# Performance work log

Hardware: AMD Instinct MI355X
Metric: run time of the kernel (lower is better)

The kernel has to match this reference:

```python
import jax, jax.numpy as jnp
import numpy as np

NUM_GRAPHS = 512
LEAKY_SLOPE = 0.01


def _gconv(x, src, dst, w, W_root, W_rel, b_rel):
    # PyG GraphConv: out = lin_rel(sum_j w_ij * x_j) + lin_root(x)
    msg = x[src] * w[:, None]                       # [E, d] gather + scale
    agg = jax.ops.segment_sum(msg, dst, num_segments=x.shape[0])  # scatter-add
    return agg @ W_rel + b_rel + x @ W_root


def setup_inputs() -> dict:
    key = jax.random.key(0)
    ks = jax.random.split(key, 12)
    N, E, D, H, C = 100000, 1250000, 64, 64, 8
    x_embeddings = jax.random.normal(ks[0], (N, D), dtype=jnp.float32)
    edge_index = jax.random.randint(ks[1], (2, E), 0, N, dtype=jnp.int64)
    weights = jax.random.uniform(ks[2], (E,), dtype=jnp.float32)
    batch = jnp.sort(jax.random.randint(ks[3], (N,), 0, NUM_GRAPHS, dtype=jnp.int64))
    s1 = 1.0 / np.sqrt(D)
    s2 = 1.0 / np.sqrt(H)
    W1_root = jax.random.uniform(ks[4], (D, H), jnp.float32, -s1, s1)
    W1_rel = jax.random.uniform(ks[5], (D, H), jnp.float32, -s1, s1)
    b1 = jax.random.uniform(ks[6], (H,), jnp.float32, -s1, s1)
    W2_root = jax.random.uniform(ks[7], (H, H), jnp.float32, -s2, s2)
    W2_rel = jax.random.uniform(ks[8], (H, H), jnp.float32, -s2, s2)
    b2 = jax.random.uniform(ks[9], (H,), jnp.float32, -s2, s2)
    Wl_root = jax.random.uniform(ks[10], (H, C), jnp.float32, -s2, s2)
    bl = jax.random.uniform(ks[11], (C,), jnp.float32, -s2, s2)
    return {"x_embeddings": x_embeddings, "edge_index": edge_index,
            "weights": weights, "batch": batch,
            "W1_root": W1_root, "W1_rel": W1_rel, "b1": b1,
            "W2_root": W2_root, "W2_rel": W2_rel, "b2": b2,
            "Wl_root": Wl_root, "bl": bl}


def reference(x_embeddings, edge_index, weights, batch,
              W1_root, W1_rel, b1, W2_root, W2_rel, b2, Wl_root, bl):
    src, dst = edge_index[0], edge_index[1]
    x = _gconv(x_embeddings, src, dst, weights, W1_root, W1_rel, b1)
    x = jax.nn.leaky_relu(x, LEAKY_SLOPE)
    x = _gconv(x, src, dst, weights, W2_root, W2_rel, b2)
    x = jax.nn.leaky_relu(x, LEAKY_SLOPE)
    # global_mean_pool over graph ids
    summed = jax.ops.segment_sum(x, batch, num_segments=NUM_GRAPHS)
    counts = jax.ops.segment_sum(jnp.ones((x.shape[0],), x.dtype), batch,
                                 num_segments=NUM_GRAPHS)
    pooled = summed / jnp.maximum(counts, 1.0)[:, None]
    # final GraphConv applied with no edges: agg = 0 -> W_root x + b_rel
    out = pooled @ Wl_root + bl
    return out
```

## Files before the change

### kernel.cpp

```cpp
#include <hip/hip_runtime.h>

#define LEAKY_SLOPE 0.01f
#define NUM_GRAPHS 512
#define TILE 4096
#define NB_MAX 512

typedef __attribute__((ext_vector_type(8))) short short8;
typedef __attribute__((ext_vector_type(4))) float f32x4;

static __device__ __forceinline__ unsigned short f2bf(float f) {
    unsigned u = __float_as_uint(f);
    u += 0x7FFFu + ((u >> 16) & 1u);
    return (unsigned short)(u >> 16);
}
static __device__ __forceinline__ float bf2f(unsigned short h) {
    return __uint_as_float(((unsigned)h) << 16);
}

static __device__ __forceinline__ int wave_incl_scan(int v, int lane) {
#pragma unroll
    for (int off = 1; off < 64; off <<= 1) {
        int t = __shfl_up(v, off, 64);
        if (lane >= off) v += t;
    }
    return v;
}

__global__ __launch_bounds__(256)
void p1a_hist(const int* __restrict__ dst, int* __restrict__ bucketCnt, int E, int NB) {
    __shared__ int h[NB_MAX];
    for (int t = threadIdx.x; t < NB_MAX; t += 256) h[t] = 0;
    __syncthreads();
    const int base = blockIdx.x * TILE;
#pragma unroll
    for (int i = 0; i < TILE / 256; ++i) {
        int e = base + i * 256 + threadIdx.x;
        if (e < E) atomicAdd(&h[dst[e] >> 8], 1);
    }
    __syncthreads();
    for (int t = threadIdx.x; t < NB; t += 256)
        if (h[t]) atomicAdd(&bucketCnt[t], h[t]);
}

__global__ __launch_bounds__(512)
void bscan_kernel(const int* __restrict__ bucketCnt, int* __restrict__ bucketBase,
                  int* __restrict__ cursor, int* __restrict__ rowStart,
                  int N, int E, int NB) {
    __shared__ int ws[8];
    const int t = threadIdx.x, lane = t & 63, wid = t >> 6;
    int v = (t < NB) ? bucketCnt[t] : 0;
    int s = wave_incl_scan(v, lane);
    if (lane == 63) ws[wid] = s;
    __syncthreads();
    int add = 0;
    for (int i = 0; i < wid; ++i) add += ws[i];
    if (t < NB) {
        int excl = s + add - v;
        bucketBase[t] = excl;
        cursor[t] = excl;
    }
    if (t == 0) rowStart[N] = E;
}

__global__ __launch_bounds__(256)
void p1b_partition(const int* __restrict__ src, const int* __restrict__ dst,
                   const float* __restrict__ w, int* __restrict__ cursor,
                   int2* __restrict__ tmp, int E, int NB) {
    __shared__ int h[NB_MAX];
    __shared__ int cur[NB_MAX];
    __shared__ int lstart[NB_MAX];
    __shared__ int gbase[NB_MAX];
    __shared__ int ws[4];
    __shared__ int2 pay[TILE];
    __shared__ unsigned short bk[TILE];

    for (int t = threadIdx.x; t < NB_MAX; t += 256) h[t] = 0;
    __syncthreads();

    const int base = blockIdx.x * TILE;
    int   myb[TILE / 256];
    int   myp[TILE / 256];
    float myw[TILE / 256];
#pragma unroll
    for (int i = 0; i < TILE / 256; ++i) {
        int e = base + i * 256 + threadIdx.x;
        if (e < E) {
            int d = dst[e];
            myb[i] = d >> 8;
            myp[i] = src[e] | ((d & 255) << 20);
            myw[i] = w[e];
            atomicAdd(&h[myb[i]], 1);
        } else {
            myb[i] = -1;
        }
    }
    __syncthreads();

    {
        const int t = threadIdx.x, lane = t & 63, wid = t >> 6;
        int a = h[2 * t], b = h[2 * t + 1];
        int s = wave_incl_scan(a + b, lane);
        if (lane == 63) ws[wid] = s;
        __syncthreads();
        int add = 0;
        for (int i = 0; i < wid; ++i) add += ws[i];
        int excl = s + add - (a + b);
        lstart[2 * t] = excl;
        lstart[2 * t + 1] = excl + a;
        cur[2 * t] = excl;
        cur[2 * t + 1] = excl + a;
    }
    __syncthreads();

#pragma unroll
    for (int i = 0; i < TILE / 256; ++i) {
        if (myb[i] >= 0) {
            int p = atomicAdd(&cur[myb[i]], 1);
            pay[p] = make_int2(myp[i], __float_as_int(myw[i]));
            bk[p] = (unsigned short)myb[i];
        }
    }
    __syncthreads();

    for (int t = threadIdx.x; t < NB; t += 256) {
        int c = h[t];
        if (c) gbase[t] = atomicAdd(&cursor[t], c);
    }
    __syncthreads();

    const int total = min(TILE, E - base);
    for (int s2 = threadIdx.x; s2 < total; s2 += 256) {
        int b2 = bk[s2];
        tmp[gbase[b2] + s2 - lstart[b2]] = pay[s2];
    }
}

__global__ __launch_bounds__(256)
void p2_build(const int2* __restrict__ tmp, const int* __restrict__ bucketBase,
              int* __restrict__ rowStart, int2* __restrict__ edata,
              int N, int E, int NB) {
    const int b = blockIdx.x;
    const int s = bucketBase[b];
    const int e2 = (b + 1 < NB) ? bucketBase[b + 1] : E;
    __shared__ int h[256];
    __shared__ int cur[256];
    __shared__ int ws[4];
    h[threadIdx.x] = 0;
    __syncthreads();
    for (int j = s + threadIdx.x; j < e2; j += 256) {
        int dl = (tmp[j].x >> 20) & 255;
        atomicAdd(&h[dl], 1);
    }
    __syncthreads();
    const int t = threadIdx.x, lane = t & 63, wid = t >> 6;
    int v = h[t];
    int sc = wave_incl_scan(v, lane);
    if (lane == 63) ws[wid] = sc;
    __syncthreads();
    int add = 0;
    for (int i = 0; i < wid; ++i) add += ws[i];
    int excl = sc + add - v;
    const int node = b * 256 + t;
    if (node < N) rowStart[node] = s + excl;
    cur[t] = excl;
    __syncthreads();
    for (int j = s + threadIdx.x; j < e2; j += 256) {
        int2 v2 = tmp[j];
        int dl = (v2.x >> 20) & 255;
        int p = atomicAdd(&cur[dl], 1);
        edata[s + p] = make_int2(v2.x & 0x1FFFF, v2.y);
    }
}

__global__ __launch_bounds__(256)
void prep_x_kernel(const float* __restrict__ x, unsigned short* __restrict__ xB, int n2) {
    int i = blockIdx.x * blockDim.x + threadIdx.x;
    if (i < n2) {
        float2 f = ((const float2*)x)[i];
        ushort2 o = make_ushort2(f2bf(f.x), f2bf(f.y));
        ((ushort2*)xB)[i] = o;
    }
}

__global__ __launch_bounds__(256)
void prep_B_kernel(const float* __restrict__ W1rel, const float* __restrict__ W1root,
                   const float* __restrict__ W2rel, const float* __restrict__ W2root,
                   unsigned short* __restrict__ Bt1, unsigned short* __restrict__ Bt2) {
    int idx = blockIdx.x * blockDim.x + threadIdx.x;
    if (idx < 2 * 64 * 128) {
        int which = idx >> 13;
        int j = idx & 8191;
        int n = j >> 7, k = j & 127;
        const float* Wr = which ? W2rel : W1rel;
        const float* Wo = which ? W2root : W1root;
        float v = (k < 64) ? Wr[k * 64 + n] : Wo[(k - 64) * 64 + n];
        (which ? Bt2 : Bt1)[j] = f2bf(v);
    }
}

__global__ __launch_bounds__(256)
void gather_kernel(const unsigned short* __restrict__ xB, const int* __restrict__ rowStart,
                   const int2* __restrict__ edata, unsigned short* __restrict__ aggB, int N) {
    const int node = blockIdx.x * 4 + (threadIdx.x >> 6);
    if (node >= N) return;
    const int lane = threadIdx.x & 63;
    const int grp  = lane >> 4;
    const int f4   = (lane & 15) * 4;
    const int s = rowStart[node];
    const int e = rowStart[node + 1];

    float a0 = 0.f, a1 = 0.f, a2 = 0.f, a3 = 0.f;
    for (int j = s; j < e; j += 8) {
        const int eA = j + grp;
        const int eB = j + 4 + grp;
        const bool vA = eA < e;
        const bool vB = eB < e;
        int2 edA = edata[vA ? eA : s];
        int2 edB = edata[vB ? eB : s];
        const float wA = vA ? __int_as_float(edA.y) : 0.0f;
        const float wB = vB ? __int_as_float(edB.y) : 0.0f;
        ushort4 rA = *(const ushort4*)(xB + (size_t)edA.x * 64 + f4);
        ushort4 rB = *(const ushort4*)(xB + (size_t)edB.x * 64 + f4);
        a0 += bf2f(rA.x) * wA;  a1 += bf2f(rA.y) * wA;
        a2 += bf2f(rA.z) * wA;  a3 += bf2f(rA.w) * wA;
        a0 += bf2f(rB.x) * wB;  a1 += bf2f(rB.y) * wB;
        a2 += bf2f(rB.z) * wB;  a3 += bf2f(rB.w) * wB;
    }
    a0 += __shfl_xor(a0, 16, 64);  a1 += __shfl_xor(a1, 16, 64);
    a2 += __shfl_xor(a2, 16, 64);  a3 += __shfl_xor(a3, 16, 64);
    a0 += __shfl_xor(a0, 32, 64);  a1 += __shfl_xor(a1, 32, 64);
    a2 += __shfl_xor(a2, 32, 64);  a3 += __shfl_xor(a3, 32, 64);
    if (grp == 0) {
        ushort4 o = make_ushort4(f2bf(a0), f2bf(a1), f2bf(a2), f2bf(a3));
        *(ushort4*)(aggB + (size_t)node * 64 + f4) = o;
    }
}

template <bool POOL>
__global__ __launch_bounds__(256)
void mfma_transform(const unsigned short* __restrict__ aggB,
                    const unsigned short* __restrict__ rootB,
                    const unsigned short* __restrict__ Bt,
                    const float* __restrict__ bias,
                    unsigned short* __restrict__ xoutB,
                    const int* __restrict__ batch,
                    float* __restrict__ pooled, int N) {
    const int wave = threadIdx.x >> 6;
    const int lane = threadIdx.x & 63;
    const int quad = lane >> 4;
    const int l16  = lane & 15;
    const int m0   = blockIdx.x * 128 + wave * 32;

    short8 bf[4][4];
#pragma unroll
    for (int t = 0; t < 4; ++t)
#pragma unroll
        for (int k = 0; k < 4; ++k)
            bf[t][k] = *(const short8*)(Bt + (t * 16 + l16) * 128 + k * 32 + quad * 8);

    f32x4 acc[2][4];
#pragma unroll
    for (int s = 0; s < 2; ++s)
#pragma unroll
        for (int t = 0; t < 4; ++t)
            acc[s][t] = (f32x4){0.f, 0.f, 0.f, 0.f};

#pragma unroll
    for (int s = 0; s < 2; ++s) {
        int row = m0 + s * 16 + l16;
        int rowc = row < N ? row : N - 1;
        const unsigned short* arow = aggB  + (size_t)rowc * 64;
        const unsigned short* xrow = rootB + (size_t)rowc * 64;
        short8 af[4];
        af[0] = *(const short8*)(arow + quad * 8);
        af[1] = *(const short8*)(arow + 32 + quad * 8);
        af[2] = *(const short8*)(xrow + quad * 8);
        af[3] = *(const short8*)(xrow + 32 + quad * 8);
#pragma unroll
        for (int t = 0; t < 4; ++t)
#pragma unroll
            for (int k = 0; k < 4; ++k)
                acc[s][t] = __builtin_amdgcn_mfma_f32_16x16x32_bf16(af[k], bf[t][k],
                                                                    acc[s][t], 0, 0, 0);
    }

#pragma unroll
    for (int s = 0; s < 2; ++s) {
#pragma unroll
        for (int t = 0; t < 4; ++t) {
            const int col = t * 16 + l16;
            const float b = bias[col];
            const int rowbase = m0 + s * 16 + quad * 4;
            if (!POOL) {
#pragma unroll
                for (int r = 0; r < 4; ++r) {
                    int row = rowbase + r;
                    if (row < N) {
                        float v = acc[s][t][r] + b;
                        v = (v > 0.0f) ? v : LEAKY_SLOPE * v;
                        xoutB[(size_t)row * 64 + col] = f2bf(v);
                    }
                }
            } else {
                float v[4]; int g[4]; int nv = 0;
#pragma unroll
                for (int r = 0; r < 4; ++r) {
                    int row = rowbase + r;
                    if (row < N) {
                        float a = acc[s][t][r] + b;
                        a = (a > 0.0f) ? a : LEAKY_SLOPE * a;
                        v[nv] = a;
                        g[nv] = batch[row];
                        ++nv;
                    }
                }
                if (nv == 4 && g[0] == g[3]) {
                    atomicAdd(&pooled[g[0] * 64 + col], v[0] + v[1] + v[2] + v[3]);
                } else {
                    for (int r = 0; r < nv; ++r)
                        atomicAdd(&pooled[g[r] * 64 + col], v[r]);
                }
            }
        }
    }
}

__global__ __launch_bounds__(64)
void final_kernel(const float* __restrict__ pooled, const int* __restrict__ batch,
                  int N, const float* __restrict__ Wl, const float* __restrict__ bl,
                  float* __restrict__ out) {
    const int g = blockIdx.x;
    const int j = threadIdx.x;
    __shared__ float sp[64];
    __shared__ int scnt;
    if (j == 0) {
        int lo = 0, hi = N;
        while (lo < hi) { int mid = (lo + hi) >> 1; if (batch[mid] < g) lo = mid + 1; else hi = mid; }
        const int start = lo;
        hi = N;
        while (lo < hi) { int mid = (lo + hi) >> 1; if (batch[mid] < g + 1) lo = mid + 1; else hi = mid; }
        scnt = lo - start;
    }
    __syncthreads();
    const float c = fmaxf((float)scnt, 1.0f);
    sp[j] = pooled[g * 64 + j] / c;
    __syncthreads();
    if (j < 8) {
        float acc = bl[j];
#pragma unroll
        for (int k = 0; k < 64; ++k) acc += sp[k] * Wl[k * 8 + j];
        out[g * 8 + j] = acc;
    }
}

extern "C" void kernel_launch(void* const* d_in, const int* in_sizes, int n_in,
                              void* d_out, int out_size, void* d_ws, size_t ws_size,
                              hipStream_t stream) {
    const float* x      = (const float*)d_in[0];
    const int*   ei     = (const int*)  d_in[1];
    const float* w      = (const float*)d_in[2];
    const int*   batch  = (const int*)  d_in[3];
    const float* W1root = (const float*)d_in[4];
    const float* W1rel  = (const float*)d_in[5];
    const float* b1     = (const float*)d_in[6];
    const float* W2root = (const float*)d_in[7];
    const float* W2rel  = (const float*)d_in[8];
    const float* b2     = (const float*)d_in[9];
    const float* Wl     = (const float*)d_in[10];
    const float* bl     = (const float*)d_in[11];
    float* out = (float*)d_out;

    const int E = in_sizes[2];
    const int N = in_sizes[3];
    const int* src = ei;
    const int* dst = ei + E;
    const int NB = (N + 255) / 256;

    unsigned short* xB   = (unsigned short*)d_ws;
    unsigned short* aggB = xB   + (size_t)N * 64;
    unsigned short* x1B  = aggB + (size_t)N * 64;
    int2*  tmp      = (int2*)(x1B + (size_t)N * 64);
    int2*  edata    = tmp + E;
    unsigned short* Bt1 = (unsigned short*)(edata + E);
    unsigned short* Bt2 = Bt1 + 64 * 128;
    int*   rowStart = (int*)(Bt2 + 64 * 128);
    int*   bucketCnt  = rowStart + (N + 1);
    int*   bucketBase = bucketCnt + NB_MAX;
    int*   cursor     = bucketBase + NB_MAX;
    float* pooled   = (float*)(cursor + NB_MAX);

    const int PB = (E + TILE - 1) / TILE;

    hipMemsetAsync(bucketCnt, 0, NB_MAX * sizeof(int), stream);
    hipMemsetAsync(pooled, 0, (size_t)NUM_GRAPHS * 64 * sizeof(float), stream);
    p1a_hist<<<PB, 256, 0, stream>>>(dst, bucketCnt, E, NB);
    prep_x_kernel<<<(N * 32 + 255) / 256, 256, 0, stream>>>(x, xB, N * 32);
    prep_B_kernel<<<64, 256, 0, stream>>>(W1rel, W1root, W2rel, W2root, Bt1, Bt2);
    bscan_kernel<<<1, 512, 0, stream>>>(bucketCnt, bucketBase, cursor, rowStart, N, E, NB);
    p1b_partition<<<PB, 256, 0, stream>>>(src, dst, w, cursor, tmp, E, NB);
    p2_build<<<NB, 256, 0, stream>>>(tmp, bucketBase, rowStart, edata, N, E, NB);

    const int tBlocks = (N + 127) / 128;
    gather_kernel<<<(N + 3) / 4, 256, 0, stream>>>(xB, rowStart, edata, aggB, N);
    mfma_transform<false><<<tBlocks, 256, 0, stream>>>(aggB, xB, Bt1, b1, x1B,
                                                       nullptr, nullptr, N);
    gather_kernel<<<(N + 3) / 4, 256, 0, stream>>>(x1B, rowStart, edata, aggB, N);
    mfma_transform<true><<<tBlocks, 256, 0, stream>>>(aggB, x1B, Bt2, b2, nullptr,
                                                      batch, pooled, N);
    final_kernel<<<NUM_GRAPHS, 64, 0, stream>>>(pooled, batch, N, Wl, bl, out);
}
```

Baseline: 298.7 us.

## Fuse prep kernels, merge memsets, vectorize transform stores and gather branches

Merges histogram, x-to-bf16 conversion and weight packing into one launch, and collapses two memsets into one over contiguous buffers. Halves the histogram/partition tile for more blocks and vectorizes the x conversion. Swaps MFMA operands in the first transform so each lane writes four contiguous bf16 outputs instead of scalar stores. Replaces clamped loads with branches in the gather loop to skip dead loads for invalid edges.

After: 322.6 us. +8.0%, slower.

```diff
diff --git a/kernel.cpp b/kernel.cpp
--- a/kernel.cpp
+++ b/kernel.cpp
@@ -2,7 +2,7 @@
 
 #define LEAKY_SLOPE 0.01f
 #define NUM_GRAPHS 512
-#define TILE 4096
+#define TILE 2048
 #define NB_MAX 512
 
 typedef __attribute__((ext_vector_type(8))) short short8;
@@ -27,19 +27,46 @@
 }
 
 __global__ __launch_bounds__(256)
-void p1a_hist(const int* __restrict__ dst, int* __restrict__ bucketCnt, int E, int NB) {
-    __shared__ int h[NB_MAX];
-    for (int t = threadIdx.x; t < NB_MAX; t += 256) h[t] = 0;
-    __syncthreads();
-    const int base = blockIdx.x * TILE;
-#pragma unroll
-    for (int i = 0; i < TILE / 256; ++i) {
-        int e = base + i * 256 + threadIdx.x;
-        if (e < E) atomicAdd(&h[dst[e] >> 8], 1);
-    }
-    __syncthreads();
-    for (int t = threadIdx.x; t < NB; t += 256)
-        if (h[t]) atomicAdd(&bucketCnt[t], h[t]);
+void mega_prep(const int* __restrict__ dst, int* __restrict__ bucketCnt, int E,
+               int NB, int histBlocks,
+               const float* __restrict__ x, unsigned short* __restrict__ xB,
+               int xElems , int xBlocks,
+               const float* __restrict__ W1rel, const float* __restrict__ W1root,
+               const float* __restrict__ W2rel, const float* __restrict__ W2root,
+               unsigned short* __restrict__ Bt1, unsigned short* __restrict__ Bt2) {
+    const int bid = blockIdx.x;
+    if (bid < histBlocks) {
+        __shared__ int h[NB_MAX];
+        for (int t = threadIdx.x; t < NB_MAX; t += 256) h[t] = 0;
+        __syncthreads();
+        const int base = bid * TILE;
+#pragma unroll
+        for (int i = 0; i < TILE / 256; ++i) {
+            int e = base + i * 256 + threadIdx.x;
+            if (e < E) atomicAdd(&h[dst[e] >> 8], 1);
+        }
+        __syncthreads();
+        for (int t = threadIdx.x; t < NB; t += 256)
+            if (h[t]) atomicAdd(&bucketCnt[t], h[t]);
+    } else if (bid < histBlocks + xBlocks) {
+        int i = (bid - histBlocks) * 256 + threadIdx.x;
+        if (i < xElems) {
+            float4 f = ((const float4*)x)[i];
+            ushort4 o = make_ushort4(f2bf(f.x), f2bf(f.y), f2bf(f.z), f2bf(f.w));
+            ((ushort4*)xB)[i] = o;
+        }
+    } else {
+        int b2 = bid - histBlocks - xBlocks;
+        for (int idx = b2 * 2048 + threadIdx.x; idx < (b2 + 1) * 2048; idx += 256) {
+            int which = idx >> 13;
+            int j = idx & 8191;
+            int n = j >> 7, k = j & 127;
+            const float* Wr = which ? W2rel : W1rel;
+            const float* Wo = which ? W2root : W1root;
+            float v = (k < 64) ? Wr[k * 64 + n] : Wo[(k - 64) * 64 + n];
+            (which ? Bt2 : Bt1)[j] = f2bf(v);
+        }
+    }
 }
 
 __global__ __launch_bounds__(512)
@@ -173,32 +200,6 @@
 }
 
 __global__ __launch_bounds__(256)
-void prep_x_kernel(const float* __restrict__ x, unsigned short* __restrict__ xB, int n2) {
-    int i = blockIdx.x * blockDim.x + threadIdx.x;
-    if (i < n2) {
-        float2 f = ((const float2*)x)[i];
-        ushort2 o = make_ushort2(f2bf(f.x), f2bf(f.y));
-        ((ushort2*)xB)[i] = o;
-    }
-}
-
-__global__ __launch_bounds__(256)
-void prep_B_kernel(const float* __restrict__ W1rel, const float* __restrict__ W1root,
-                   const float* __restrict__ W2rel, const float* __restrict__ W2root,
-                   unsigned short* __restrict__ Bt1, unsigned short* __restrict__ Bt2) {
-    int idx = blockIdx.x * blockDim.x + threadIdx.x;
-    if (idx < 2 * 64 * 128) {
-        int which = idx >> 13;
-        int j = idx & 8191;
-        int n = j >> 7, k = j & 127;
-        const float* Wr = which ? W2rel : W1rel;
-        const float* Wo = which ? W2root : W1root;
-        float v = (k < 64) ? Wr[k * 64 + n] : Wo[(k - 64) * 64 + n];
-        (which ? Bt2 : Bt1)[j] = f2bf(v);
-    }
-}
-
-__global__ __launch_bounds__(256)
 void gather_kernel(const unsigned short* __restrict__ xB, const int* __restrict__ rowStart,
                    const int2* __restrict__ edata, unsigned short* __restrict__ aggB, int N) {
     const int node = blockIdx.x * 4 + (threadIdx.x >> 6);
@@ -212,19 +213,21 @@
     float a0 = 0.f, a1 = 0.f, a2 = 0.f, a3 = 0.f;
     for (int j = s; j < e; j += 8) {
         const int eA = j + grp;
-        const int eB = j + 4 + grp;
-        const bool vA = eA < e;
-        const bool vB = eB < e;
-        int2 edA = edata[vA ? eA : s];
-        int2 edB = edata[vB ? eB : s];
-        const float wA = vA ? __int_as_float(edA.y) : 0.0f;
-        const float wB = vB ? __int_as_float(edB.y) : 0.0f;
-        ushort4 rA = *(const ushort4*)(xB + (size_t)edA.x * 64 + f4);
-        ushort4 rB = *(const ushort4*)(xB + (size_t)edB.x * 64 + f4);
-        a0 += bf2f(rA.x) * wA;  a1 += bf2f(rA.y) * wA;
-        a2 += bf2f(rA.z) * wA;  a3 += bf2f(rA.w) * wA;
-        a0 += bf2f(rB.x) * wB;  a1 += bf2f(rB.y) * wB;
-        a2 += bf2f(rB.z) * wB;  a3 += bf2f(rB.w) * wB;
+        const int eB = eA + 4;
+        if (eA < e) {
+            int2 ed = edata[eA];
+            float wv = __int_as_float(ed.y);
+            ushort4 r = *(const ushort4*)(xB + (size_t)ed.x * 64 + f4);
+            a0 += bf2f(r.x) * wv;  a1 += bf2f(r.y) * wv;
+            a2 += bf2f(r.z) * wv;  a3 += bf2f(r.w) * wv;
+        }
+        if (eB < e) {
+            int2 ed = edata[eB];
+            float wv = __int_as_float(ed.y);
+            ushort4 r = *(const ushort4*)(xB + (size_t)ed.x * 64 + f4);
+            a0 += bf2f(r.x) * wv;  a1 += bf2f(r.y) * wv;
+            a2 += bf2f(r.z) * wv;  a3 += bf2f(r.w) * wv;
+        }
     }
     a0 += __shfl_xor(a0, 16, 64);  a1 += __shfl_xor(a1, 16, 64);
     a2 += __shfl_xor(a2, 16, 64);  a3 += __shfl_xor(a3, 16, 64);
@@ -236,15 +239,12 @@
     }
 }
 
-template <bool POOL>
-__global__ __launch_bounds__(256)
-void mfma_transform(const unsigned short* __restrict__ aggB,
-                    const unsigned short* __restrict__ rootB,
-                    const unsigned short* __restrict__ Bt,
-                    const float* __restrict__ bias,
-                    unsigned short* __restrict__ xoutB,
-                    const int* __restrict__ batch,
-                    float* __restrict__ pooled, int N) {
+__global__ __launch_bounds__(256)
+void transform_store(const unsigned short* __restrict__ aggB,
+                     const unsigned short* __restrict__ rootB,
+                     const unsigned short* __restrict__ Bt,
+                     const float* __restrict__ bias,
+                     unsigned short* __restrict__ xoutB, int N) {
     const int wave = threadIdx.x >> 6;
     const int lane = threadIdx.x & 63;
     const int quad = lane >> 4;
@@ -280,6 +280,74 @@
         for (int t = 0; t < 4; ++t)
 #pragma unroll
             for (int k = 0; k < 4; ++k)
+                acc[s][t] = __builtin_amdgcn_mfma_f32_16x16x32_bf16(bf[t][k], af[k],
+                                                                    acc[s][t], 0, 0, 0);
+    }
+
+#pragma unroll
+    for (int s = 0; s < 2; ++s) {
+        const int node = m0 + s * 16 + l16;
+        if (node < N) {
+#pragma unroll
+            for (int t = 0; t < 4; ++t) {
+                const float4 bb = *(const float4*)(bias + t * 16 + quad * 4);
+                float v0 = acc[s][t][0] + bb.x;
+                float v1 = acc[s][t][1] + bb.y;
+                float v2 = acc[s][t][2] + bb.z;
+                float v3 = acc[s][t][3] + bb.w;
+                v0 = (v0 > 0.f) ? v0 : LEAKY_SLOPE * v0;
+                v1 = (v1 > 0.f) ? v1 : LEAKY_SLOPE * v1;
+                v2 = (v2 > 0.f) ? v2 : LEAKY_SLOPE * v2;
+                v3 = (v3 > 0.f) ? v3 : LEAKY_SLOPE * v3;
+                ushort4 o = make_ushort4(f2bf(v0), f2bf(v1), f2bf(v2), f2bf(v3));
+                *(ushort4*)(xoutB + (size_t)node * 64 + t * 16 + quad * 4) = o;
+            }
+        }
+    }
+}
+
+__global__ __launch_bounds__(256)
+void transform_pool(const unsigned short* __restrict__ aggB,
+                    const unsigned short* __restrict__ rootB,
+                    const unsigned short* __restrict__ Bt,
+                    const float* __restrict__ bias,
+                    const int* __restrict__ batch,
+                    float* __restrict__ pooled, int N) {
+    const int wave = threadIdx.x >> 6;
+    const int lane = threadIdx.x & 63;
+    const int quad = lane >> 4;
+    const int l16  = lane & 15;
+    const int m0   = blockIdx.x * 128 + wave * 32;
+
+    short8 bf[4][4];
+#pragma unroll
+    for (int t = 0; t < 4; ++t)
+#pragma unroll
+        for (int k = 0; k < 4; ++k)
+            bf[t][k] = *(const short8*)(Bt + (t * 16 + l16) * 128 + k * 32 + quad * 8);
+
+    f32x4 acc[2][4];
+#pragma unroll
+    for (int s = 0; s < 2; ++s)
+#pragma unroll
+        for (int t = 0; t < 4; ++t)
+            acc[s][t] = (f32x4){0.f, 0.f, 0.f, 0.f};
+
+#pragma unroll
+    for (int s = 0; s < 2; ++s) {
+        int row = m0 + s * 16 + l16;
+        int rowc = row < N ? row : N - 1;
+        const unsigned short* arow = aggB  + (size_t)rowc * 64;
+        const unsigned short* xrow = rootB + (size_t)rowc * 64;
+        short8 af[4];
+        af[0] = *(const short8*)(arow + quad * 8);
+        af[1] = *(const short8*)(arow + 32 + quad * 8);
+        af[2] = *(const short8*)(xrow + quad * 8);
+        af[3] = *(const short8*)(xrow + 32 + quad * 8);
+#pragma unroll
+        for (int t = 0; t < 4; ++t)
+#pragma unroll
+            for (int k = 0; k < 4; ++k)
                 acc[s][t] = __builtin_amdgcn_mfma_f32_16x16x32_bf16(af[k], bf[t][k],
                                                                     acc[s][t], 0, 0, 0);
     }
@@ -291,35 +359,23 @@
             const int col = t * 16 + l16;
             const float b = bias[col];
             const int rowbase = m0 + s * 16 + quad * 4;
-            if (!POOL) {
-#pragma unroll
-                for (int r = 0; r < 4; ++r) {
-                    int row = rowbase + r;
-                    if (row < N) {
-                        float v = acc[s][t][r] + b;
-                        v = (v > 0.0f) ? v : LEAKY_SLOPE * v;
-                        xoutB[(size_t)row * 64 + col] = f2bf(v);
-                    }
+            float v[4]; int g[4]; int nv = 0;
+#pragma unroll
+            for (int r = 0; r < 4; ++r) {
+                int row = rowbase + r;
+                if (row < N) {
+                    float a = acc[s][t][r] + b;
+                    a = (a > 0.0f) ? a : LEAKY_SLOPE * a;
+                    v[nv] = a;
+                    g[nv] = batch[row];
+                    ++nv;
                 }
+            }
+            if (nv == 4 && g[0] == g[3]) {
+                atomicAdd(&pooled[g[0] * 64 + col], v[0] + v[1] + v[2] + v[3]);
             } else {
-                float v[4]; int g[4]; int nv = 0;
-#pragma unroll
-                for (int r = 0; r < 4; ++r) {
-                    int row = rowbase + r;
-                    if (row < N) {
-                        float a = acc[s][t][r] + b;
-                        a = (a > 0.0f) ? a : LEAKY_SLOPE * a;
-                        v[nv] = a;
-                        g[nv] = batch[row];
-                        ++nv;
-                    }
-                }
-                if (nv == 4 && g[0] == g[3]) {
-                    atomicAdd(&pooled[g[0] * 64 + col], v[0] + v[1] + v[2] + v[3]);
-                } else {
-                    for (int r = 0; r < nv; ++r)
-                        atomicAdd(&pooled[g[r] * 64 + col], v[r]);
-                }
+                for (int r = 0; r < nv; ++r)
+                    atomicAdd(&pooled[g[r] * 64 + col], v[r]);
             }
         }
     }
@@ -389,23 +445,23 @@
     int*   cursor     = bucketBase + NB_MAX;
     float* pooled   = (float*)(cursor + NB_MAX);
 
-    const int PB = (E + TILE - 1) / TILE;
-
-    hipMemsetAsync(bucketCnt, 0, NB_MAX * sizeof(int), stream);
-    hipMemsetAsync(pooled, 0, (size_t)NUM_GRAPHS * 64 * sizeof(float), stream);
-    p1a_hist<<<PB, 256, 0, stream>>>(dst, bucketCnt, E, NB);
-    prep_x_kernel<<<(N * 32 + 255) / 256, 256, 0, stream>>>(x, xB, N * 32);
-    prep_B_kernel<<<64, 256, 0, stream>>>(W1rel, W1root, W2rel, W2root, Bt1, Bt2);
+    const int histBlocks = (E + TILE - 1) / TILE;
+    const int xElems = N * 16;
+    const int xBlocks = (xElems + 255) / 256;
+
+    hipMemsetAsync(bucketCnt, 0, (3 * NB_MAX + NUM_GRAPHS * 64) * sizeof(float), stream);
+    mega_prep<<<histBlocks + xBlocks + 8, 256, 0, stream>>>(
+        dst, bucketCnt, E, NB, histBlocks,
+        x, xB, xElems, xBlocks,
+        W1rel, W1root, W2rel, W2root, Bt1, Bt2);
     bscan_kernel<<<1, 512, 0, stream>>>(bucketCnt, bucketBase, cursor, rowStart, N, E, NB);
-    p1b_partition<<<PB, 256, 0, stream>>>(src, dst, w, cursor, tmp, E, NB);
+    p1b_partition<<<histBlocks, 256, 0, stream>>>(src, dst, w, cursor, tmp, E, NB);
     p2_build<<<NB, 256, 0, stream>>>(tmp, bucketBase, rowStart, edata, N, E, NB);
 
     const int tBlocks = (N + 127) / 128;
     gather_kernel<<<(N + 3) / 4, 256, 0, stream>>>(xB, rowStart, edata, aggB, N);
-    mfma_transform<false><<<tBlocks, 256, 0, stream>>>(aggB, xB, Bt1, b1, x1B,
-                                                       nullptr, nullptr, N);
+    transform_store<<<tBlocks, 256, 0, stream>>>(aggB, xB, Bt1, b1, x1B, N);
     gather_kernel<<<(N + 3) / 4, 256, 0, stream>>>(x1B, rowStart, edata, aggB, N);
-    mfma_transform<true><<<tBlocks, 256, 0, stream>>>(aggB, x1B, Bt2, b2, nullptr,
-                                                      batch, pooled, N);
+    transform_pool<<<tBlocks, 256, 0, stream>>>(aggB, x1B, Bt2, b2, batch, pooled, N);
     final_kernel<<<NUM_GRAPHS, 64, 0, stream>>>(pooled, batch, N, Wl, bl, out);
 }
```
